# Kernel tuning notes

Hardware: AMD Instinct MI355X
Metric: run time of the kernel (lower is better)

The kernel has to match this reference:

```python
import jax, jax.numpy as jnp
import numpy as np

BN_EPS = 1e-5
LEAKY_SLOPE = 0.2


def setup_inputs() -> dict:
    key = jax.random.key(0)
    k1, k2, k3 = jax.random.split(key, 3)
    B, C, N, K, CO = 4, 64, 16384, 16, 64
    x = jax.random.normal(k1, (B, C, N, 1), dtype=jnp.float32)
    edge_index = jax.random.randint(k2, (B, N, K), 0, N)  # neighbor ids per point
    W = jax.random.normal(k3, (CO, 2 * C), dtype=jnp.float32) * 0.05  # 1x1 conv weight [out, 2*in]
    gamma = jnp.ones((CO,), dtype=jnp.float32)
    beta = jnp.zeros((CO,), dtype=jnp.float32)
    return {"x": x, "edge_index": edge_index, "W": W, "gamma": gamma, "beta": beta}


def reference(x, edge_index, W, gamma, beta):
    # x: [B, C, N, 1], edge_index: [B, N, K], W: [CO, 2C]
    B, C, N, _ = x.shape
    xc = x[..., 0]                      # [B, C, N]
    xt = xc.transpose(0, 2, 1)          # [B, N, C]
    # batched gather of neighbor features: x_j [B, C, N, K]
    x_j = jax.vmap(lambda xb, ib: xb[ib])(xt, edge_index)  # [B, N, K, C]
    x_j = x_j.transpose(0, 3, 1, 2)
    # conv(concat([x_i, x_i - x_j])) == (W1 + W2) @ x_i  -  W2 @ x_j  (1x1 conv, no bias)
    W1, W2 = W[:, :C], W[:, C:]
    h = jnp.einsum('oc,bcn->bon', W1 + W2, xc)[..., None] \
        - jnp.einsum('oc,bcnk->bonk', W2, x_j)            # [B, CO, N, K]
    # BatchNorm2d (training-mode batch statistics, biased variance as in torch)
    mean = h.mean(axis=(0, 2, 3))
    var = h.var(axis=(0, 2, 3))
    hn = (h - mean[None, :, None, None]) * jax.lax.rsqrt(var + BN_EPS)[None, :, None, None]
    hbn = gamma[None, :, None, None] * hn + beta[None, :, None, None]
    a = jnp.where(hbn >= 0, hbn, LEAKY_SLOPE * hbn)
    # max aggregation over neighbors, keepdim -> [B, CO, N, 1]
    return jnp.max(a, axis=3, keepdims=True)
```

## Files before the change

### kernel.cpp

```cpp
#include <hip/hip_runtime.h>
#include <hip/hip_bf16.h>
#include <stdint.h>

#define NDIM 16384
#define KNB 16
#define BNK_F 1048576.0f

union Pack4 { __hip_bfloat16 h[4]; uint2 u; };

__global__ __launch_bounds__(256) void gemm_y_kernel(
    const float* __restrict__ x,
    const float* __restrict__ W,
    __hip_bfloat16* __restrict__ y1,
    __hip_bfloat16* __restrict__ y2,
    float* __restrict__ stats)
{
    __shared__ alignas(16) unsigned int lds_w[64 * 68];
    __shared__ alignas(16) float        lds_x[64 * 68];

    const int tid = threadIdx.x;
    if (blockIdx.x == 0 && tid < 128) stats[tid] = 0.0f;

    const int b  = blockIdx.x >> 8;
    const int n0 = (blockIdx.x & 255) << 6;

    for (int i = tid; i < 4096; i += 256) {
        int c = i & 63, o = i >> 6;
        float w1 = W[o * 128 + c];
        float w2 = W[o * 128 + 64 + c];
        unsigned int u12 = (unsigned int)__bfloat16_as_ushort(__float2bfloat16(w1 + w2));
        unsigned int u2  = (unsigned int)__bfloat16_as_ushort(__float2bfloat16(w2));
        lds_w[c * 68 + o] = u12 | (u2 << 16);
    }
    const float* xb = x + (size_t)b * 64 * NDIM + n0;
    for (int i = tid; i < 4096; i += 256) {
        int nl = i & 63, c = i >> 6;
        lds_x[c * 68 + nl] = xb[(size_t)c * NDIM + nl];
    }
    __syncthreads();

    const int o0  = (tid & 15) * 4;
    const int nl0 = (tid >> 4) * 4;
    float acc1[4][4] = {}, acc2[4][4] = {};
    #pragma unroll 4
    for (int c = 0; c < 64; ++c) {
        float4 xv = *(const float4*)&lds_x[c * 68 + nl0];
        uint4  wv = *(const uint4*)&lds_w[c * 68 + o0];
        const float xa[4] = { xv.x, xv.y, xv.z, xv.w };
        const unsigned int wu[4] = { wv.x, wv.y, wv.z, wv.w };
        #pragma unroll
        for (int j = 0; j < 4; ++j) {
            float w12 = __uint_as_float(wu[j] << 16);
            float w2f = __uint_as_float(wu[j] & 0xffff0000u);
            #pragma unroll
            for (int i = 0; i < 4; ++i) {
                acc1[i][j] = fmaf(w12, xa[i], acc1[i][j]);
                acc2[i][j] = fmaf(w2f, xa[i], acc2[i][j]);
            }
        }
    }
    const size_t bn0 = (size_t)b * NDIM + n0;
    #pragma unroll
    for (int i = 0; i < 4; ++i) {
        Pack4 p1, p2;
        #pragma unroll
        for (int j = 0; j < 4; ++j) {
            p1.h[j] = __float2bfloat16(acc1[i][j]);
            p2.h[j] = __float2bfloat16(acc2[i][j]);
        }
        size_t off = (bn0 + nl0 + i) * 64 + o0;
        *(uint2*)(y1 + off) = p1.u;
        *(uint2*)(y2 + off) = p2.u;
    }
}

__global__ __launch_bounds__(256, 4) void gather_kernel(
    const unsigned* __restrict__ y1p,
    const unsigned* __restrict__ y2p,
    const int* __restrict__ ei,
    const float* __restrict__ gamma,
    unsigned* __restrict__ hselp,
    float* __restrict__ partials)
{
    const int tid  = threadIdx.x;
    const int w    = __builtin_amdgcn_readfirstlane(tid >> 6);
    const int lane = tid & 63;
    const int half = lane >> 5;
    const int c2   = lane & 31;
    const int g    = blockIdx.x;
    const int xcd  = g & 7;
    const int b    = xcd >> 1;
    const int hlf  = xcd & 1;
    const int lb   = g >> 3;
    const int row0 = b * NDIM + hlf * 8192 + lb * 32 + w * 8;

    const unsigned sgn0 = (gamma[2 * c2]     >= 0.0f) ? 0x80000000u : 0u;
    const unsigned sgn1 = (gamma[2 * c2 + 1] >= 0.0f) ? 0x80000000u : 0u;
    const unsigned* y2b = y2p + ((size_t)b * NDIM) * 32 + c2;

    float ssum0 = 0.f, ssum1 = 0.f, ssq0 = 0.f, ssq1 = 0.f;

    for (int rp = 0; rp < 8; rp += 2) {
        const int ra = row0 + rp;
        const int* iA = ei + (size_t)ra * KNB;
        const int* iB = ei + (size_t)(ra + 1) * KNB;

        unsigned u[KNB];
        #pragma unroll
        for (int k = 0; k < KNB; ++k) {
            int j = half ? iB[k] : iA[k];
            u[k] = y2b[(size_t)j * 32];
        }
        const unsigned y1u = y1p[(size_t)(ra + half) * 32 + c2];

        float s20 = 0.f, s21 = 0.f, q20 = 0.f, q21 = 0.f;
        float M0 = -3.402823e38f, M1 = -3.402823e38f;
        #pragma unroll
        for (int k = 0; k < KNB; ++k) {
            unsigned lo = u[k] << 16;
            unsigned hi = u[k] & 0xffff0000u;
            float v0 = __uint_as_float(lo);
            float v1 = __uint_as_float(hi);
            s20 += v0;               s21 += v1;
            q20 = fmaf(v0, v0, q20); q21 = fmaf(v1, v1, q21);
            M0 = fmaxf(M0, __uint_as_float(lo ^ sgn0));
            M1 = fmaxf(M1, __uint_as_float(hi ^ sgn1));
        }
        const float y1lo = __uint_as_float(y1u << 16);
        const float y1hi = __uint_as_float(y1u & 0xffff0000u);
        const float e0 = __uint_as_float(__float_as_uint(M0) ^ sgn0);
        const float e1 = __uint_as_float(__float_as_uint(M1) ^ sgn1);
        const float h0 = y1lo - e0;
        const float h1 = y1hi - e1;
        unsigned pk = (unsigned)__bfloat16_as_ushort(__float2bfloat16(h0))
                    | ((unsigned)__bfloat16_as_ushort(__float2bfloat16(h1)) << 16);
        hselp[(size_t)(ra + half) * 32 + c2] = pk;
        ssum0 += 16.f * y1lo - s20;
        ssum1 += 16.f * y1hi - s21;
        ssq0  += fmaf(fmaf(-2.f, s20, 16.f * y1lo), y1lo, q20);
        ssq1  += fmaf(fmaf(-2.f, s21, 16.f * y1hi), y1hi, q21);
    }

    __shared__ float rs[8][64];
    __shared__ float rq[8][64];
    rs[w * 2 + half][c2 * 2]     = ssum0;
    rs[w * 2 + half][c2 * 2 + 1] = ssum1;
    rq[w * 2 + half][c2 * 2]     = ssq0;
    rq[w * 2 + half][c2 * 2 + 1] = ssq1;
    __syncthreads();
    if (tid < 128) {
        const int c = tid & 63;
        float v = 0.f;
        if (tid < 64) {
            #pragma unroll
            for (int r = 0; r < 8; ++r) v += rs[r][c];
        } else {
            #pragma unroll
            for (int r = 0; r < 8; ++r) v += rq[r][c];
        }
        partials[(size_t)g * 128 + tid] = v;
    }
}

__global__ __launch_bounds__(256) void reduce_kernel(
    const float* __restrict__ partials,
    float* __restrict__ stats)
{
    __shared__ float lds[256];
    const int tid = threadIdx.x;
    const int c   = tid & 127;
    const int q   = tid >> 7;
    const int r0  = blockIdx.x * 32 + q * 16;
    float acc = 0.f;
    #pragma unroll
    for (int r = 0; r < 16; ++r)
        acc += partials[(size_t)(r0 + r) * 128 + c];
    lds[tid] = acc;
    __syncthreads();
    if (tid < 128) atomicAdd(&stats[tid], lds[tid] + lds[tid + 128]);
}

__global__ __launch_bounds__(256) void out_kernel(
    const unsigned* __restrict__ hselp,
    const float* __restrict__ stats,
    const float* __restrict__ gamma,
    const float* __restrict__ beta,
    float* __restrict__ out)
{
    __shared__ float tile[64 * 65];
    __shared__ float sc[64], bi[64];
    const int tid = threadIdx.x;
    if (tid < 64) {
        float mean = stats[tid] * (1.0f / BNK_F);
        float var  = stats[64 + tid] * (1.0f / BNK_F) - mean * mean;
        float s    = gamma[tid] * rsqrtf(var + 1e-5f);
        sc[tid] = s;
        bi[tid] = beta[tid] - mean * s;
    }
    __syncthreads();

    const int b  = blockIdx.x >> 8;
    const int n0 = (blockIdx.x & 255) << 6;
    const size_t bn0 = (size_t)b * NDIM + n0;
    const int c2 = tid & 31;
    const int r0 = tid >> 5;

    for (int r = r0; r < 64; r += 8) {
        unsigned u = hselp[(bn0 + r) * 32 + c2];
        float v0 = fmaf(sc[2 * c2],     __uint_as_float(u << 16),          bi[2 * c2]);
        float v1 = fmaf(sc[2 * c2 + 1], __uint_as_float(u & 0xffff0000u), bi[2 * c2 + 1]);
        v0 = (v0 >= 0.f) ? v0 : 0.2f * v0;
        v1 = (v1 >= 0.f) ? v1 : 0.2f * v1;
        tile[r * 65 + 2 * c2]     = v0;
        tile[r * 65 + 2 * c2 + 1] = v1;
    }
    __syncthreads();
    const int lane = tid & 63;
    for (int o = tid >> 6; o < 64; o += 4)
        out[((size_t)(b * 64 + o) << 14) + n0 + lane] = tile[lane * 65 + o];
}

extern "C" void kernel_launch(void* const* d_in, const int* in_sizes, int n_in,
                              void* d_out, int out_size, void* d_ws, size_t ws_size,
                              hipStream_t stream) {
    const float* x     = (const float*)d_in[0];
    const int*   ei    = (const int*)d_in[1];
    const float* W     = (const float*)d_in[2];
    const float* gamma = (const float*)d_in[3];
    const float* beta  = (const float*)d_in[4];
    float* out = (float*)d_out;

    char* ws = (char*)d_ws;
    __hip_bfloat16* y1    = (__hip_bfloat16*)(ws);
    __hip_bfloat16* y2    = (__hip_bfloat16*)(ws + 8388608);
    unsigned*       hselp = (unsigned*)(ws + 16777216);
    float*          part  = (float*)(ws + 25165824);
    float*          stats = (float*)(ws + 25165824 + 1048576);

    gemm_y_kernel <<<dim3(1024), dim3(256), 0, stream>>>(x, W, y1, y2, stats);
    gather_kernel <<<dim3(2048), dim3(256), 0, stream>>>((const unsigned*)y1, (const unsigned*)y2,
                                                         ei, gamma, hselp, part);
    reduce_kernel <<<dim3(64),   dim3(256), 0, stream>>>(part, stats);
    out_kernel    <<<dim3(1024), dim3(256), 0, stream>>>(hselp, stats, gamma, beta, out);
}
```

Measured before the change: 115.0 us.

## Fuse all four stages into one cooperative kernel with grid syncs

Replaces the four separate launches (GEMM, gather, reduce, output) with a single persistent cooperative kernel that uses grid.sync between stages, removing per-launch gaps. Each block owns 64 rows across all stages, so the gather now handles 16 rows per wave instead of 8. The x tile is also packed to bf16 in LDS, which cuts LDS footprint and may change GEMM rounding. The cost is three grid-wide barriers and an occupancy check on every call, with a fallback to the old multi-kernel path if the cooperative launch is unavailable.

After: 117.0 us. No clear change (+1.7%).

```diff
diff --git a/kernel.cpp b/kernel.cpp
--- a/kernel.cpp
+++ b/kernel.cpp
@@ -1,6 +1,9 @@
 #include <hip/hip_runtime.h>
 #include <hip/hip_bf16.h>
+#include <hip/hip_cooperative_groups.h>
 #include <stdint.h>
+
+namespace cg = cooperative_groups;
 
 #define NDIM 16384
 #define KNB 16
@@ -8,29 +11,202 @@
 
 union Pack4 { __hip_bfloat16 h[4]; uint2 u; };
 
+__device__ inline unsigned pack_bf16(float a, float b) {
+    return (unsigned)__bfloat16_as_ushort(__float2bfloat16(a))
+         | ((unsigned)__bfloat16_as_ushort(__float2bfloat16(b)) << 16);
+}
+
+__global__ __launch_bounds__(256, 4) void fused_all(
+    const float* __restrict__ x,
+    const int* __restrict__ ei,
+    const float* __restrict__ W,
+    const float* __restrict__ gamma,
+    const float* __restrict__ beta,
+    float* __restrict__ out,
+    unsigned* __restrict__ y1p,
+    unsigned* __restrict__ y2p,
+    unsigned* __restrict__ hselp,
+    float* __restrict__ partials,
+    float* __restrict__ stats)
+{
+    __shared__ alignas(16) unsigned char smem[26112];
+    __shared__ float sc[64], bi[64];
+    unsigned* lds_w  = (unsigned*)smem;
+    unsigned* lds_xp = (unsigned*)(smem + 17408);
+    float*    lds_f  = (float*)smem;
+
+    cg::grid_group grid = cg::this_grid();
+    const int tid  = threadIdx.x;
+    const int g    = blockIdx.x;
+    const int xcd  = g & 7;
+    const int b    = xcd >> 1;
+    const int n0   = (xcd & 1) * 8192 + (g >> 3) * 64;
+    const int row0 = b * NDIM + n0;
+
+    if (g == 0 && tid < 128) stats[tid] = 0.0f;
+
+    for (int i = tid; i < 4096; i += 256) {
+        int c = i & 63, o = i >> 6;
+        float w1 = W[o * 128 + c];
+        float w2 = W[o * 128 + 64 + c];
+        lds_w[c * 68 + o] = pack_bf16(w1 + w2, w2);
+    }
+    const float* xb = x + (size_t)b * 64 * NDIM + n0;
+    for (int i = tid; i < 2048; i += 256) {
+        int np = i & 31, c = i >> 5;
+        const float2 xv = *(const float2*)(xb + (size_t)c * NDIM + 2 * np);
+        lds_xp[c * 34 + np] = pack_bf16(xv.x, xv.y);
+    }
+    __syncthreads();
+    {
+        const int o0  = (tid & 15) * 4;
+        const int nl0 = (tid >> 4) * 4;
+        float acc1[4][4] = {}, acc2[4][4] = {};
+        #pragma unroll 4
+        for (int c = 0; c < 64; ++c) {
+            uint2 xv = *(const uint2*)&lds_xp[c * 34 + (nl0 >> 1)];
+            uint4 wv = *(const uint4*)&lds_w[c * 68 + o0];
+            const float xa[4] = { __uint_as_float(xv.x << 16), __uint_as_float(xv.x & 0xffff0000u),
+                                  __uint_as_float(xv.y << 16), __uint_as_float(xv.y & 0xffff0000u) };
+            const unsigned wu[4] = { wv.x, wv.y, wv.z, wv.w };
+            #pragma unroll
+            for (int j = 0; j < 4; ++j) {
+                float w12 = __uint_as_float(wu[j] << 16);
+                float w2f = __uint_as_float(wu[j] & 0xffff0000u);
+                #pragma unroll
+                for (int i = 0; i < 4; ++i) {
+                    acc1[i][j] = fmaf(w12, xa[i], acc1[i][j]);
+                    acc2[i][j] = fmaf(w2f, xa[i], acc2[i][j]);
+                }
+            }
+        }
+        #pragma unroll
+        for (int i = 0; i < 4; ++i) {
+            uint2 p1 = { pack_bf16(acc1[i][0], acc1[i][1]), pack_bf16(acc1[i][2], acc1[i][3]) };
+            uint2 p2 = { pack_bf16(acc2[i][0], acc2[i][1]), pack_bf16(acc2[i][2], acc2[i][3]) };
+            size_t off = (size_t)(row0 + nl0 + i) * 32 + (o0 >> 1);
+            *(uint2*)&y1p[off] = p1;
+            *(uint2*)&y2p[off] = p2;
+        }
+    }
+    grid.sync();
+
+    const int w    = __builtin_amdgcn_readfirstlane(tid >> 6);
+    const int lane = tid & 63;
+    const int half = lane >> 5;
+    const int c2   = lane & 31;
+    const unsigned sgn0 = (gamma[2 * c2]     >= 0.0f) ? 0x80000000u : 0u;
+    const unsigned sgn1 = (gamma[2 * c2 + 1] >= 0.0f) ? 0x80000000u : 0u;
+    const unsigned* y2b = y2p + ((size_t)b * NDIM) * 32 + c2;
+
+    float ssum0 = 0.f, ssum1 = 0.f, ssq0 = 0.f, ssq1 = 0.f;
+    const int wrow0 = row0 + w * 16;
+    for (int rp = 0; rp < 16; rp += 2) {
+        const int ra = wrow0 + rp;
+        const int* iA = ei + (size_t)ra * KNB;
+        const int* iB = ei + (size_t)(ra + 1) * KNB;
+
+        unsigned u[KNB];
+        #pragma unroll
+        for (int k = 0; k < KNB; ++k) {
+            int j = half ? iB[k] : iA[k];
+            u[k] = y2b[(size_t)j * 32];
+        }
+        const unsigned y1u = y1p[(size_t)(ra + half) * 32 + c2];
+
+        float s20 = 0.f, s21 = 0.f, q20 = 0.f, q21 = 0.f;
+        float M0 = -3.402823e38f, M1 = -3.402823e38f;
+        #pragma unroll
+        for (int k = 0; k < KNB; ++k) {
+            unsigned lo = u[k] << 16;
+            unsigned hi = u[k] & 0xffff0000u;
+            float v0 = __uint_as_float(lo);
+            float v1 = __uint_as_float(hi);
+            s20 += v0;               s21 += v1;
+            q20 = fmaf(v0, v0, q20); q21 = fmaf(v1, v1, q21);
+            M0 = fmaxf(M0, __uint_as_float(lo ^ sgn0));
+            M1 = fmaxf(M1, __uint_as_float(hi ^ sgn1));
+        }
+        const float y1lo = __uint_as_float(y1u << 16);
+        const float y1hi = __uint_as_float(y1u & 0xffff0000u);
+        const float h0 = y1lo - __uint_as_float(__float_as_uint(M0) ^ sgn0);
+        const float h1 = y1hi - __uint_as_float(__float_as_uint(M1) ^ sgn1);
+        hselp[(size_t)(ra + half) * 32 + c2] = pack_bf16(h0, h1);
+        ssum0 += 16.f * y1lo - s20;
+        ssum1 += 16.f * y1hi - s21;
+        ssq0  += fmaf(fmaf(-2.f, s20, 16.f * y1lo), y1lo, q20);
+        ssq1  += fmaf(fmaf(-2.f, s21, 16.f * y1hi), y1hi, q21);
+    }
+    {
+        float* rs = lds_f;
+        float* rq = lds_f + 512;
+        rs[(w * 2 + half) * 64 + c2 * 2]     = ssum0;
+        rs[(w * 2 + half) * 64 + c2 * 2 + 1] = ssum1;
+        rq[(w * 2 + half) * 64 + c2 * 2]     = ssq0;
+        rq[(w * 2 + half) * 64 + c2 * 2 + 1] = ssq1;
+        __syncthreads();
+        if (tid < 128) {
+            const int c = tid & 63;
+            float v = 0.f;
+            const float* src = (tid < 64) ? rs : rq;
+            #pragma unroll
+            for (int r = 0; r < 8; ++r) v += src[r * 64 + c];
+            partials[(size_t)g * 128 + tid] = v;
+        }
+    }
+    grid.sync();
+
+    if (g < 64) {
+        const int c = tid & 127;
+        const int r0 = g * 16 + (tid >> 7) * 8;
+        float acc = 0.f;
+        #pragma unroll
+        for (int r = 0; r < 8; ++r)
+            acc += partials[(size_t)(r0 + r) * 128 + c];
+        lds_f[tid] = acc;
+        __syncthreads();
+        if (tid < 128) atomicAdd(&stats[tid], lds_f[tid] + lds_f[tid + 128]);
+    }
+    grid.sync();
+
+    if (tid < 64) {
+        float mean = stats[tid] * (1.0f / BNK_F);
+        float var  = stats[64 + tid] * (1.0f / BNK_F) - mean * mean;
+        float s    = gamma[tid] * rsqrtf(var + 1e-5f);
+        sc[tid] = s;
+        bi[tid] = beta[tid] - mean * s;
+    }
+    __syncthreads();
+    float* tile = lds_f;
+    for (int r = tid >> 5; r < 64; r += 8) {
+        unsigned u = hselp[(size_t)(row0 + r) * 32 + c2];
+        float v0 = fmaf(sc[2 * c2],     __uint_as_float(u << 16),          bi[2 * c2]);
+        float v1 = fmaf(sc[2 * c2 + 1], __uint_as_float(u & 0xffff0000u), bi[2 * c2 + 1]);
+        v0 = (v0 >= 0.f) ? v0 : 0.2f * v0;
+        v1 = (v1 >= 0.f) ? v1 : 0.2f * v1;
+        tile[r * 65 + 2 * c2]     = v0;
+        tile[r * 65 + 2 * c2 + 1] = v1;
+    }
+    __syncthreads();
+    for (int o = tid >> 6; o < 64; o += 4)
+        out[((size_t)(b * 64 + o) << 14) + n0 + lane] = tile[lane * 65 + o];
+}
+
 __global__ __launch_bounds__(256) void gemm_y_kernel(
-    const float* __restrict__ x,
-    const float* __restrict__ W,
-    __hip_bfloat16* __restrict__ y1,
-    __hip_bfloat16* __restrict__ y2,
+    const float* __restrict__ x, const float* __restrict__ W,
+    __hip_bfloat16* __restrict__ y1, __hip_bfloat16* __restrict__ y2,
     float* __restrict__ stats)
 {
     __shared__ alignas(16) unsigned int lds_w[64 * 68];
     __shared__ alignas(16) float        lds_x[64 * 68];
-
     const int tid = threadIdx.x;
     if (blockIdx.x == 0 && tid < 128) stats[tid] = 0.0f;
-
     const int b  = blockIdx.x >> 8;
     const int n0 = (blockIdx.x & 255) << 6;
-
     for (int i = tid; i < 4096; i += 256) {
         int c = i & 63, o = i >> 6;
-        float w1 = W[o * 128 + c];
-        float w2 = W[o * 128 + 64 + c];
-        unsigned int u12 = (unsigned int)__bfloat16_as_ushort(__float2bfloat16(w1 + w2));
-        unsigned int u2  = (unsigned int)__bfloat16_as_ushort(__float2bfloat16(w2));
-        lds_w[c * 68 + o] = u12 | (u2 << 16);
+        float w1 = W[o * 128 + c], w2 = W[o * 128 + 64 + c];
+        lds_w[c * 68 + o] = pack_bf16(w1 + w2, w2);
     }
     const float* xb = x + (size_t)b * 64 * NDIM + n0;
     for (int i = tid; i < 4096; i += 256) {
@@ -38,7 +214,6 @@
         lds_x[c * 68 + nl] = xb[(size_t)c * NDIM + nl];
     }
     __syncthreads();
-
     const int o0  = (tid & 15) * 4;
     const int nl0 = (tid >> 4) * 4;
     float acc1[4][4] = {}, acc2[4][4] = {};
@@ -47,7 +222,7 @@
         float4 xv = *(const float4*)&lds_x[c * 68 + nl0];
         uint4  wv = *(const uint4*)&lds_w[c * 68 + o0];
         const float xa[4] = { xv.x, xv.y, xv.z, xv.w };
-        const unsigned int wu[4] = { wv.x, wv.y, wv.z, wv.w };
+        const unsigned wu[4] = { wv.x, wv.y, wv.z, wv.w };
         #pragma unroll
         for (int j = 0; j < 4; ++j) {
             float w12 = __uint_as_float(wu[j] << 16);
@@ -75,12 +250,9 @@
 }
 
 __global__ __launch_bounds__(256, 4) void gather_kernel(
-    const unsigned* __restrict__ y1p,
-    const unsigned* __restrict__ y2p,
-    const int* __restrict__ ei,
-    const float* __restrict__ gamma,
-    unsigned* __restrict__ hselp,
-    float* __restrict__ partials)
+    const unsigned* __restrict__ y1p, const unsigned* __restrict__ y2p,
+    const int* __restrict__ ei, const float* __restrict__ gamma,
+    unsigned* __restrict__ hselp, float* __restrict__ partials)
 {
     const int tid  = threadIdx.x;
     const int w    = __builtin_amdgcn_readfirstlane(tid >> 6);
@@ -90,21 +262,15 @@
     const int g    = blockIdx.x;
     const int xcd  = g & 7;
     const int b    = xcd >> 1;
-    const int hlf  = xcd & 1;
-    const int lb   = g >> 3;
-    const int row0 = b * NDIM + hlf * 8192 + lb * 32 + w * 8;
-
+    const int row0 = b * NDIM + (xcd & 1) * 8192 + (g >> 3) * 32 + w * 8;
     const unsigned sgn0 = (gamma[2 * c2]     >= 0.0f) ? 0x80000000u : 0u;
     const unsigned sgn1 = (gamma[2 * c2 + 1] >= 0.0f) ? 0x80000000u : 0u;
     const unsigned* y2b = y2p + ((size_t)b * NDIM) * 32 + c2;
-
     float ssum0 = 0.f, ssum1 = 0.f, ssq0 = 0.f, ssq1 = 0.f;
-
     for (int rp = 0; rp < 8; rp += 2) {
         const int ra = row0 + rp;
         const int* iA = ei + (size_t)ra * KNB;
         const int* iB = ei + (size_t)(ra + 1) * KNB;
-
         unsigned u[KNB];
         #pragma unroll
         for (int k = 0; k < KNB; ++k) {
@@ -112,15 +278,12 @@
             u[k] = y2b[(size_t)j * 32];
         }
         const unsigned y1u = y1p[(size_t)(ra + half) * 32 + c2];
-
         float s20 = 0.f, s21 = 0.f, q20 = 0.f, q21 = 0.f;
         float M0 = -3.402823e38f, M1 = -3.402823e38f;
         #pragma unroll
         for (int k = 0; k < KNB; ++k) {
-            unsigned lo = u[k] << 16;
-            unsigned hi = u[k] & 0xffff0000u;
-            float v0 = __uint_as_float(lo);
-            float v1 = __uint_as_float(hi);
+            unsigned lo = u[k] << 16, hi = u[k] & 0xffff0000u;
+            float v0 = __uint_as_float(lo), v1 = __uint_as_float(hi);
             s20 += v0;               s21 += v1;
             q20 = fmaf(v0, v0, q20); q21 = fmaf(v1, v1, q21);
             M0 = fmaxf(M0, __uint_as_float(lo ^ sgn0));
@@ -128,19 +291,14 @@
         }
         const float y1lo = __uint_as_float(y1u << 16);
         const float y1hi = __uint_as_float(y1u & 0xffff0000u);
-        const float e0 = __uint_as_float(__float_as_uint(M0) ^ sgn0);
-        const float e1 = __uint_as_float(__float_as_uint(M1) ^ sgn1);
-        const float h0 = y1lo - e0;
-        const float h1 = y1hi - e1;
-        unsigned pk = (unsigned)__bfloat16_as_ushort(__float2bfloat16(h0))
-                    | ((unsigned)__bfloat16_as_ushort(__float2bfloat16(h1)) << 16);
-        hselp[(size_t)(ra + half) * 32 + c2] = pk;
+        const float h0 = y1lo - __uint_as_float(__float_as_uint(M0) ^ sgn0);
+        const float h1 = y1hi - __uint_as_float(__float_as_uint(M1) ^ sgn1);
+        hselp[(size_t)(ra + half) * 32 + c2] = pack_bf16(h0, h1);
         ssum0 += 16.f * y1lo - s20;
         ssum1 += 16.f * y1hi - s21;
         ssq0  += fmaf(fmaf(-2.f, s20, 16.f * y1lo), y1lo, q20);
         ssq1  += fmaf(fmaf(-2.f, s21, 16.f * y1hi), y1hi, q21);
     }
-
     __shared__ float rs[8][64];
     __shared__ float rq[8][64];
     rs[w * 2 + half][c2 * 2]     = ssum0;
@@ -151,26 +309,19 @@
     if (tid < 128) {
         const int c = tid & 63;
         float v = 0.f;
-        if (tid < 64) {
-            #pragma unroll
-            for (int r = 0; r < 8; ++r) v += rs[r][c];
-        } else {
-            #pragma unroll
-            for (int r = 0; r < 8; ++r) v += rq[r][c];
-        }
+        if (tid < 64) { for (int r = 0; r < 8; ++r) v += rs[r][c]; }
+        else          { for (int r = 0; r < 8; ++r) v += rq[r][c]; }
         partials[(size_t)g * 128 + tid] = v;
     }
 }
 
 __global__ __launch_bounds__(256) void reduce_kernel(
-    const float* __restrict__ partials,
-    float* __restrict__ stats)
+    const float* __restrict__ partials, float* __restrict__ stats)
 {
     __shared__ float lds[256];
     const int tid = threadIdx.x;
     const int c   = tid & 127;
-    const int q   = tid >> 7;
-    const int r0  = blockIdx.x * 32 + q * 16;
+    const int r0  = blockIdx.x * 32 + (tid >> 7) * 16;
     float acc = 0.f;
     #pragma unroll
     for (int r = 0; r < 16; ++r)
@@ -181,10 +332,8 @@
 }
 
 __global__ __launch_bounds__(256) void out_kernel(
-    const unsigned* __restrict__ hselp,
-    const float* __restrict__ stats,
-    const float* __restrict__ gamma,
-    const float* __restrict__ beta,
+    const unsigned* __restrict__ hselp, const float* __restrict__ stats,
+    const float* __restrict__ gamma, const float* __restrict__ beta,
     float* __restrict__ out)
 {
     __shared__ float tile[64 * 65];
@@ -198,14 +347,11 @@
         bi[tid] = beta[tid] - mean * s;
     }
     __syncthreads();
-
     const int b  = blockIdx.x >> 8;
     const int n0 = (blockIdx.x & 255) << 6;
     const size_t bn0 = (size_t)b * NDIM + n0;
     const int c2 = tid & 31;
-    const int r0 = tid >> 5;
-
-    for (int r = r0; r < 64; r += 8) {
+    for (int r = tid >> 5; r < 64; r += 8) {
         unsigned u = hselp[(bn0 + r) * 32 + c2];
         float v0 = fmaf(sc[2 * c2],     __uint_as_float(u << 16),          bi[2 * c2]);
         float v1 = fmaf(sc[2 * c2 + 1], __uint_as_float(u & 0xffff0000u), bi[2 * c2 + 1]);
@@ -231,15 +377,27 @@
     float* out = (float*)d_out;
 
     char* ws = (char*)d_ws;
-    __hip_bfloat16* y1    = (__hip_bfloat16*)(ws);
-    __hip_bfloat16* y2    = (__hip_bfloat16*)(ws + 8388608);
-    unsigned*       hselp = (unsigned*)(ws + 16777216);
-    float*          part  = (float*)(ws + 25165824);
-    float*          stats = (float*)(ws + 25165824 + 1048576);
-
-    gemm_y_kernel <<<dim3(1024), dim3(256), 0, stream>>>(x, W, y1, y2, stats);
-    gather_kernel <<<dim3(2048), dim3(256), 0, stream>>>((const unsigned*)y1, (const unsigned*)y2,
-                                                         ei, gamma, hselp, part);
+    unsigned* y1p   = (unsigned*)(ws);
+    unsigned* y2p   = (unsigned*)(ws + 8388608);
+    unsigned* hselp = (unsigned*)(ws + 16777216);
+    float*    part  = (float*)(ws + 25165824);
+    float*    stats = (float*)(ws + 25165824 + 1048576);
+
+    int occ = 0;
+    hipError_t qerr = hipOccupancyMaxActiveBlocksPerMultiprocessor(
+        &occ, (const void*)fused_all, 256, 0);
+    if (qerr == hipSuccess && occ >= 4) {
+        void* kargs[] = { (void*)&x, (void*)&ei, (void*)&W, (void*)&gamma, (void*)&beta,
+                          (void*)&out, (void*)&y1p, (void*)&y2p, (void*)&hselp,
+                          (void*)&part, (void*)&stats };
+        hipError_t lerr = hipLaunchCooperativeKernel((const void*)fused_all,
+                                                     dim3(1024), dim3(256), kargs, 0, stream);
+        if (lerr == hipSuccess) return;
+    }
+
+    gemm_y_kernel <<<dim3(1024), dim3(256), 0, stream>>>(x, W, (__hip_bfloat16*)y1p,
+                                                         (__hip_bfloat16*)y2p, stats);
+    gather_kernel <<<dim3(2048), dim3(256), 0, stream>>>(y1p, y2p, ei, gamma, hselp, part);
     reduce_kernel <<<dim3(64),   dim3(256), 0, stream>>>(part, stats);
     out_kernel    <<<dim3(1024), dim3(256), 0, stream>>>(hselp, stats, gamma, beta, out);
 }
```

## Use bf16 MFMA for pointwise GEMM and fold stats reduction into gather

Applied to the files above, without the earlier changes.

Replaces the scalar FMA GEMM with bf16 MFMA 16x16x32 instructions. The x input is now rounded to bf16 before the multiply, which adds precision loss. The separate reduce kernel is removed. Gather blocks atomically accumulate into 32 striped stat slots, and the last block, found through an atomic counter, computes BN scale and bias for the output kernel. This drops one launch and the partials round trip, at the cost of atomic contention and a serialized tail in one block.

Measured after the change: 162.4 us. +41.2%, slower.

```diff
diff --git a/kernel.cpp b/kernel.cpp
--- a/kernel.cpp
+++ b/kernel.cpp
@@ -6,71 +6,73 @@
 #define KNB 16
 #define BNK_F 1048576.0f
 
-union Pack4 { __hip_bfloat16 h[4]; uint2 u; };
-
-__global__ __launch_bounds__(256) void gemm_y_kernel(
+typedef __attribute__((ext_vector_type(8))) short bf16x8_t;
+typedef __attribute__((ext_vector_type(4))) float f32x4_t;
+
+__device__ inline unsigned pack_bf16(float a, float b) {
+    return (unsigned)__bfloat16_as_ushort(__float2bfloat16(a))
+         | ((unsigned)__bfloat16_as_ushort(__float2bfloat16(b)) << 16);
+}
+
+__global__ __launch_bounds__(256) void gemm_mfma_kernel(
     const float* __restrict__ x,
     const float* __restrict__ W,
-    __hip_bfloat16* __restrict__ y1,
-    __hip_bfloat16* __restrict__ y2,
-    float* __restrict__ stats)
+    unsigned* __restrict__ y1p,
+    unsigned* __restrict__ y2p,
+    float* __restrict__ statsN,
+    unsigned* __restrict__ counter)
 {
-    __shared__ alignas(16) unsigned int lds_w[64 * 68];
-    __shared__ alignas(16) float        lds_x[64 * 68];
+    __shared__ alignas(16) short lds_a[128 * 72];
+    __shared__ alignas(16) short lds_b[64 * 72];
 
     const int tid = threadIdx.x;
-    if (blockIdx.x == 0 && tid < 128) stats[tid] = 0.0f;
-
+    if (blockIdx.x == 0) {
+        for (int i = tid; i < 4096; i += 256) statsN[i] = 0.0f;
+        if (tid == 0) *counter = 0u;
+    }
     const int b  = blockIdx.x >> 8;
     const int n0 = (blockIdx.x & 255) << 6;
 
-    for (int i = tid; i < 4096; i += 256) {
-        int c = i & 63, o = i >> 6;
-        float w1 = W[o * 128 + c];
-        float w2 = W[o * 128 + 64 + c];
-        unsigned int u12 = (unsigned int)__bfloat16_as_ushort(__float2bfloat16(w1 + w2));
-        unsigned int u2  = (unsigned int)__bfloat16_as_ushort(__float2bfloat16(w2));
-        lds_w[c * 68 + o] = u12 | (u2 << 16);
-    }
-    const float* xb = x + (size_t)b * 64 * NDIM + n0;
-    for (int i = tid; i < 4096; i += 256) {
-        int nl = i & 63, c = i >> 6;
-        lds_x[c * 68 + nl] = xb[(size_t)c * NDIM + nl];
-    }
-    __syncthreads();
-
-    const int o0  = (tid & 15) * 4;
-    const int nl0 = (tid >> 4) * 4;
-    float acc1[4][4] = {}, acc2[4][4] = {};
-    #pragma unroll 4
-    for (int c = 0; c < 64; ++c) {
-        float4 xv = *(const float4*)&lds_x[c * 68 + nl0];
-        uint4  wv = *(const uint4*)&lds_w[c * 68 + o0];
-        const float xa[4] = { xv.x, xv.y, xv.z, xv.w };
-        const unsigned int wu[4] = { wv.x, wv.y, wv.z, wv.w };
-        #pragma unroll
-        for (int j = 0; j < 4; ++j) {
-            float w12 = __uint_as_float(wu[j] << 16);
-            float w2f = __uint_as_float(wu[j] & 0xffff0000u);
-            #pragma unroll
-            for (int i = 0; i < 4; ++i) {
-                acc1[i][j] = fmaf(w12, xa[i], acc1[i][j]);
-                acc2[i][j] = fmaf(w2f, xa[i], acc2[i][j]);
-            }
-        }
-    }
-    const size_t bn0 = (size_t)b * NDIM + n0;
+    for (int i = tid; i < 8192; i += 256) {
+        int ch = i >> 6, c = i & 63;
+        float a = (ch < 64) ? (W[ch * 128 + c] + W[ch * 128 + 64 + c])
+                            : W[(ch - 64) * 128 + 64 + c];
+        lds_a[ch * 72 + c] = (short)__bfloat16_as_ushort(__float2bfloat16(a));
+    }
+    {
+        const float* xb = x + (size_t)b * 64 * NDIM + n0;
+        const int n = tid & 63;
+        unsigned* lb32 = (unsigned*)lds_b;
+        for (int cp = tid >> 6; cp < 32; cp += 4) {
+            int c = cp * 2;
+            float x0 = xb[(size_t)c * NDIM + n];
+            float x1 = xb[(size_t)(c + 1) * NDIM + n];
+            lb32[n * 36 + cp] = pack_bf16(x0, x1);
+        }
+    }
+    __syncthreads();
+
+    const int lane = tid & 63;
+    const int w    = tid >> 6;
+    const int m    = lane & 15;
+    const int q    = lane >> 4;
+    const int n    = w * 16 + m;
+
+    const bf16x8_t b0 = *(const bf16x8_t*)&lds_b[n * 72 + q * 8];
+    const bf16x8_t b1 = *(const bf16x8_t*)&lds_b[n * 72 + q * 8 + 32];
+
+    const size_t rowbase = ((size_t)(b * NDIM + n0 + n)) * 32;
     #pragma unroll
-    for (int i = 0; i < 4; ++i) {
-        Pack4 p1, p2;
-        #pragma unroll
-        for (int j = 0; j < 4; ++j) {
-            p1.h[j] = __float2bfloat16(acc1[i][j]);
-            p2.h[j] = __float2bfloat16(acc2[i][j]);
-        }
-        size_t off = (bn0 + nl0 + i) * 64 + o0;
-        *(uint2*)(y1 + off) = p1.u;
-        *(uint2*)(y2 + off) = p2.u;
+    for (int t = 0; t < 8; ++t) {
+        const short* ap = &lds_a[(t * 16 + m) * 72 + q * 8];
+        bf16x8_t a0 = *(const bf16x8_t*)ap;
+        bf16x8_t a1 = *(const bf16x8_t*)(ap + 32);
+        f32x4_t acc = {0.f, 0.f, 0.f, 0.f};
+        acc = __builtin_amdgcn_mfma_f32_16x16x32_bf16(a0, b0, acc, 0, 0, 0);
+        acc = __builtin_amdgcn_mfma_f32_16x16x32_bf16(a1, b1, acc, 0, 0, 0);
+        unsigned* dst = (t < 4) ? y1p : y2p;
+        uint2 pk = { pack_bf16(acc[0], acc[1]), pack_bf16(acc[2], acc[3]) };
+        *(uint2*)&dst[rowbase + (t & 3) * 8 + q * 2] = pk;
     }
 }
 
@@ -79,8 +81,11 @@
     const unsigned* __restrict__ y2p,
     const int* __restrict__ ei,
     const float* __restrict__ gamma,
+    const float* __restrict__ beta,
     unsigned* __restrict__ hselp,
-    float* __restrict__ partials)
+    float* __restrict__ statsN,
+    float* __restrict__ sb,
+    unsigned* __restrict__ counter)
 {
     const int tid  = threadIdx.x;
     const int w    = __builtin_amdgcn_readfirstlane(tid >> 6);
@@ -90,21 +95,17 @@
     const int g    = blockIdx.x;
     const int xcd  = g & 7;
     const int b    = xcd >> 1;
-    const int hlf  = xcd & 1;
-    const int lb   = g >> 3;
-    const int row0 = b * NDIM + hlf * 8192 + lb * 32 + w * 8;
+    const int row0 = b * NDIM + (xcd & 1) * 8192 + (g >> 3) * 32 + w * 8;
 
     const unsigned sgn0 = (gamma[2 * c2]     >= 0.0f) ? 0x80000000u : 0u;
     const unsigned sgn1 = (gamma[2 * c2 + 1] >= 0.0f) ? 0x80000000u : 0u;
     const unsigned* y2b = y2p + ((size_t)b * NDIM) * 32 + c2;
 
     float ssum0 = 0.f, ssum1 = 0.f, ssq0 = 0.f, ssq1 = 0.f;
-
     for (int rp = 0; rp < 8; rp += 2) {
         const int ra = row0 + rp;
         const int* iA = ei + (size_t)ra * KNB;
         const int* iB = ei + (size_t)(ra + 1) * KNB;
-
         unsigned u[KNB];
         #pragma unroll
         for (int k = 0; k < KNB; ++k) {
@@ -112,15 +113,12 @@
             u[k] = y2b[(size_t)j * 32];
         }
         const unsigned y1u = y1p[(size_t)(ra + half) * 32 + c2];
-
         float s20 = 0.f, s21 = 0.f, q20 = 0.f, q21 = 0.f;
         float M0 = -3.402823e38f, M1 = -3.402823e38f;
         #pragma unroll
         for (int k = 0; k < KNB; ++k) {
-            unsigned lo = u[k] << 16;
-            unsigned hi = u[k] & 0xffff0000u;
-            float v0 = __uint_as_float(lo);
-            float v1 = __uint_as_float(hi);
+            unsigned lo = u[k] << 16, hi = u[k] & 0xffff0000u;
+            float v0 = __uint_as_float(lo), v1 = __uint_as_float(hi);
             s20 += v0;               s21 += v1;
             q20 = fmaf(v0, v0, q20); q21 = fmaf(v1, v1, q21);
             M0 = fmaxf(M0, __uint_as_float(lo ^ sgn0));
@@ -128,13 +126,9 @@
         }
         const float y1lo = __uint_as_float(y1u << 16);
         const float y1hi = __uint_as_float(y1u & 0xffff0000u);
-        const float e0 = __uint_as_float(__float_as_uint(M0) ^ sgn0);
-        const float e1 = __uint_as_float(__float_as_uint(M1) ^ sgn1);
-        const float h0 = y1lo - e0;
-        const float h1 = y1hi - e1;
-        unsigned pk = (unsigned)__bfloat16_as_ushort(__float2bfloat16(h0))
-                    | ((unsigned)__bfloat16_as_ushort(__float2bfloat16(h1)) << 16);
-        hselp[(size_t)(ra + half) * 32 + c2] = pk;
+        const float h0 = y1lo - __uint_as_float(__float_as_uint(M0) ^ sgn0);
+        const float h1 = y1hi - __uint_as_float(__float_as_uint(M1) ^ sgn1);
+        hselp[(size_t)(ra + half) * 32 + c2] = pack_bf16(h0, h1);
         ssum0 += 16.f * y1lo - s20;
         ssum1 += 16.f * y1hi - s21;
         ssq0  += fmaf(fmaf(-2.f, s20, 16.f * y1lo), y1lo, q20);
@@ -143,6 +137,8 @@
 
     __shared__ float rs[8][64];
     __shared__ float rq[8][64];
+    __shared__ float colsum[128];
+    __shared__ int   isLast;
     rs[w * 2 + half][c2 * 2]     = ssum0;
     rs[w * 2 + half][c2 * 2 + 1] = ssum1;
     rq[w * 2 + half][c2 * 2]     = ssq0;
@@ -151,51 +147,48 @@
     if (tid < 128) {
         const int c = tid & 63;
         float v = 0.f;
+        if (tid < 64) { for (int r = 0; r < 8; ++r) v += rs[r][c]; }
+        else          { for (int r = 0; r < 8; ++r) v += rq[r][c]; }
+        atomicAdd(&statsN[(g & 31) * 128 + tid], v);
+    }
+    __syncthreads();
+    if (tid == 0) {
+        __threadfence();
+        isLast = (atomicAdd(counter, 1u) == 2047u);
+    }
+    __syncthreads();
+    if (isLast) {
+        __threadfence();
+        if (tid < 128) {
+            float v = 0.f;
+            #pragma unroll
+            for (int i = 0; i < 32; ++i)
+                v += __hip_atomic_load(&statsN[i * 128 + tid],
+                                       __ATOMIC_RELAXED, __HIP_MEMORY_SCOPE_AGENT);
+            colsum[tid] = v;
+        }
+        __syncthreads();
         if (tid < 64) {
-            #pragma unroll
-            for (int r = 0; r < 8; ++r) v += rs[r][c];
-        } else {
-            #pragma unroll
-            for (int r = 0; r < 8; ++r) v += rq[r][c];
-        }
-        partials[(size_t)g * 128 + tid] = v;
-    }
-}
-
-__global__ __launch_bounds__(256) void reduce_kernel(
-    const float* __restrict__ partials,
-    float* __restrict__ stats)
-{
-    __shared__ float lds[256];
-    const int tid = threadIdx.x;
-    const int c   = tid & 127;
-    const int q   = tid >> 7;
-    const int r0  = blockIdx.x * 32 + q * 16;
-    float acc = 0.f;
-    #pragma unroll
-    for (int r = 0; r < 16; ++r)
-        acc += partials[(size_t)(r0 + r) * 128 + c];
-    lds[tid] = acc;
-    __syncthreads();
-    if (tid < 128) atomicAdd(&stats[tid], lds[tid] + lds[tid + 128]);
+            float mean = colsum[tid] * (1.0f / BNK_F);
+            float var  = colsum[64 + tid] * (1.0f / BNK_F) - mean * mean;
+            float s    = gamma[tid] * rsqrtf(var + 1e-5f);
+            sb[tid]      = s;
+            sb[64 + tid] = beta[tid] - mean * s;
+        }
+    }
 }
 
 __global__ __launch_bounds__(256) void out_kernel(
     const unsigned* __restrict__ hselp,
-    const float* __restrict__ stats,
-    const float* __restrict__ gamma,
-    const float* __restrict__ beta,
+    const float* __restrict__ sb,
     float* __restrict__ out)
 {
     __shared__ float tile[64 * 65];
     __shared__ float sc[64], bi[64];
     const int tid = threadIdx.x;
-    if (tid < 64) {
-        float mean = stats[tid] * (1.0f / BNK_F);
-        float var  = stats[64 + tid] * (1.0f / BNK_F) - mean * mean;
-        float s    = gamma[tid] * rsqrtf(var + 1e-5f);
-        sc[tid] = s;
-        bi[tid] = beta[tid] - mean * s;
+    if (tid < 128) {
+        if (tid < 64) sc[tid] = sb[tid];
+        else          bi[tid - 64] = sb[tid];
     }
     __syncthreads();
 
@@ -203,9 +196,8 @@
     const int n0 = (blockIdx.x & 255) << 6;
     const size_t bn0 = (size_t)b * NDIM + n0;
     const int c2 = tid & 31;
-    const int r0 = tid >> 5;
-
-    for (int r = r0; r < 64; r += 8) {
+
+    for (int r = tid >> 5; r < 64; r += 8) {
         unsigned u = hselp[(bn0 + r) * 32 + c2];
         float v0 = fmaf(sc[2 * c2],     __uint_as_float(u << 16),          bi[2 * c2]);
         float v1 = fmaf(sc[2 * c2 + 1], __uint_as_float(u & 0xffff0000u), bi[2 * c2 + 1]);
@@ -231,15 +223,15 @@
     float* out = (float*)d_out;
 
     char* ws = (char*)d_ws;
-    __hip_bfloat16* y1    = (__hip_bfloat16*)(ws);
-    __hip_bfloat16* y2    = (__hip_bfloat16*)(ws + 8388608);
-    unsigned*       hselp = (unsigned*)(ws + 16777216);
-    float*          part  = (float*)(ws + 25165824);
-    float*          stats = (float*)(ws + 25165824 + 1048576);
-
-    gemm_y_kernel <<<dim3(1024), dim3(256), 0, stream>>>(x, W, y1, y2, stats);
-    gather_kernel <<<dim3(2048), dim3(256), 0, stream>>>((const unsigned*)y1, (const unsigned*)y2,
-                                                         ei, gamma, hselp, part);
-    reduce_kernel <<<dim3(64),   dim3(256), 0, stream>>>(part, stats);
-    out_kernel    <<<dim3(1024), dim3(256), 0, stream>>>(hselp, stats, gamma, beta, out);
-}
+    unsigned* y1p     = (unsigned*)(ws);
+    unsigned* y2p     = (unsigned*)(ws + 8388608);
+    unsigned* hselp   = (unsigned*)(ws + 16777216);
+    float*    statsN  = (float*)(ws + 25165824);
+    float*    sb      = (float*)(ws + 25165824 + 16384);
+    unsigned* counter = (unsigned*)(ws + 25165824 + 16384 + 512);
+
+    gemm_mfma_kernel <<<dim3(1024), dim3(256), 0, stream>>>(x, W, y1p, y2p, statsN, counter);
+    gather_kernel    <<<dim3(2048), dim3(256), 0, stream>>>(y1p, y2p, ei, gamma, beta,
+                                                            hselp, statsN, sb, counter);
+    out_kernel       <<<dim3(1024), dim3(256), 0, stream>>>(hselp, sb, out);
+}
```
